# Kernel tuning notes

Hardware: AMD Instinct MI355X
Metric: run time of the kernel (lower is better)

The kernel has to match this reference:

```python
import jax, jax.numpy as jnp
from jax import lax
import numpy as np

VOCAB = 100000
MAX_SEQ = 8192
DIM = 128
K = 5
STRIDE = 1
PAD = 2


def setup_inputs() -> dict:
    key = jax.random.key(0)
    ks = jax.random.split(key, 6)
    X = jax.random.randint(ks[0], (8, 8192), 0, VOCAB, dtype=jnp.int64)
    # nn.Linear(vocab, dim): weight (dim, vocab), bias (dim)
    W_lin = jax.random.normal(ks[1], (DIM, VOCAB), dtype=jnp.float32) * 0.02
    b_lin = jax.random.normal(ks[2], (DIM,), dtype=jnp.float32) * 0.02
    # nn.Conv1d(dim, dim, k): weight (out=dim, in=dim, k), bias (dim)
    W_conv = jax.random.normal(ks[3], (DIM, DIM, K), dtype=jnp.float32) * 0.02
    b_conv = jax.random.normal(ks[4], (DIM,), dtype=jnp.float32) * 0.02
    # nn.Embedding(max_seq_len, dim)
    pos_table = jax.random.normal(ks[5], (MAX_SEQ, DIM), dtype=jnp.float32) * 0.02
    return {"X": X, "W_lin": W_lin, "b_lin": b_lin,
            "W_conv": W_conv, "b_conv": b_conv, "pos_table": pos_table}


def reference(X, W_lin, b_lin, W_conv, b_conv, pos_table):
    # one_hot(X) @ W_lin.T + b_lin  ==  gather rows of W_lin.T
    emb = jnp.take(W_lin.T, X, axis=0) + b_lin          # (b, n, d)
    x = jnp.transpose(emb, (0, 2, 1))                   # (b, d, n)
    y = lax.conv_general_dilated(
        x, W_conv, window_strides=(STRIDE,), padding=[(PAD, PAD)],
        dimension_numbers=("NCH", "OIH", "NCH"))
    y = y + b_conv[None, :, None]                       # (b, d, n_out)
    tokens = jnp.transpose(y, (0, 2, 1))                # (b, n_out, d)
    n_out = tokens.shape[1]
    return tokens + pos_table[:n_out][None, :, :]
```

## Files before the change

### kernel.cpp

```cpp
#include <hip/hip_runtime.h>
#include <hip/hip_bf16.h>
#include <stdint.h>

#define VOCAB 100000
#define SEQ   8192
#define BATCH 8
#define DIM   128

typedef short bf16x8 __attribute__((ext_vector_type(8)));
typedef float f32x4  __attribute__((ext_vector_type(4)));

__device__ __forceinline__ ushort f2bf(float f) {
  union { float f; uint32_t u; } v; v.f = f;
  uint32_t u = v.u;
  return (ushort)((u + 0x7FFF + ((u >> 16) & 1)) >> 16);
}

__global__ void repack_wconv(const float* __restrict__ wconv,
                             ushort* __restrict__ wcb) {
  int e = blockIdx.x * 256 + threadIdx.x;
  if (e >= 5 * DIM * DIM) return;
  int k = e / (DIM * DIM);
  int rem = e % (DIM * DIM);
  int d = rem / DIM, i = rem % DIM;
  wcb[e] = f2bf(wconv[(d * DIM + i) * 5 + k]);
}

__global__ __launch_bounds__(256) void build_wlt(
    const float* __restrict__ wlin, const float* __restrict__ blin,
    ushort* __restrict__ wlt) {
  __shared__ float tile[128 * 65];
  const int tid = threadIdx.x;
  const int t0  = blockIdx.x * 64;

  const int c4 = (tid & 15) * 4;
  const int rbase = tid >> 4;
  const bool cvalid = (t0 + c4) < VOCAB;
#pragma unroll
  for (int p = 0; p < 8; ++p) {
    int r = p * 16 + rbase;
    float4 v = make_float4(0.f, 0.f, 0.f, 0.f);
    if (cvalid) v = *(const float4*)(wlin + (size_t)r * VOCAB + t0 + c4);
    float* dst = &tile[r * 65 + c4];
    dst[0] = v.x; dst[1] = v.y; dst[2] = v.z; dst[3] = v.w;
  }
  __syncthreads();

  const int chunk = tid & 15;
  float bias8[8];
#pragma unroll
  for (int j = 0; j < 8; ++j) bias8[j] = blin[chunk * 8 + j];

#pragma unroll
  for (int p = 0; p < 4; ++p) {
    int tl = (tid >> 4) + p * 16;
    int t  = t0 + tl;
    if (t >= VOCAB) continue;
    ushort u[8];
#pragma unroll
    for (int j = 0; j < 8; ++j) {
      float f = tile[(chunk * 8 + j) * 65 + tl] + bias8[j];
      u[j] = f2bf(f);
    }
    *(uint4*)(wlt + (size_t)t * DIM + chunk * 8) = *(const uint4*)u;
  }
}

__global__ __launch_bounds__(256, 2) void conv_main(
    const int* __restrict__ X, const ushort* __restrict__ wlt,
    const ushort* __restrict__ wcb, const float* __restrict__ bconv,
    const float* __restrict__ pos, float* __restrict__ out) {
  __shared__ __align__(16) ushort Atile[132 * 136];

  const int tid   = threadIdx.x;
  const int bm    = blockIdx.x;
  const int batch = bm >> 6;
  const int nbase = (bm & 63) << 7;
  const int* Xb   = X + batch * SEQ;

  int  tok[9];
  bool valid[9];
#pragma unroll
  for (int it = 0; it < 9; ++it) {
    int c = tid + it * 256;
    int r = c >> 4;
    int n = nbase - 2 + r;
    bool v = (c < 2112) && (n >= 0) && (n < SEQ);
    valid[it] = v;
    tok[it] = v ? Xb[n] : 0;
  }
  uint4 val[9];
#pragma unroll
  for (int it = 0; it < 9; ++it) {
    int c = tid + it * 256;
    int ch = c & 15;
    val[it] = valid[it] ? *(const uint4*)(wlt + (size_t)tok[it] * DIM + ch * 8)
                        : make_uint4(0u, 0u, 0u, 0u);
  }
#pragma unroll
  for (int it = 0; it < 9; ++it) {
    int c = tid + it * 256;
    if (c < 2112) {
      int r = c >> 4, ch = c & 15;
      *(uint4*)&Atile[r * 136 + ch * 8] = val[it];
    }
  }
  __syncthreads();

  const int wave = tid >> 6;
  const int lane = tid & 63;
  const int wm = (wave >> 1) << 6;
  const int wn = (wave & 1) << 6;
  const int lr = lane & 15;
  const int lq = lane >> 4;

  f32x4 acc[4][4];
#pragma unroll
  for (int a = 0; a < 4; ++a)
#pragma unroll
    for (int b = 0; b < 4; ++b) acc[a][b] = (f32x4)0.f;

#pragma unroll
  for (int k = 0; k < 5; ++k) {
    bf16x8 B[4][4];
#pragma unroll
    for (int nt = 0; nt < 4; ++nt)
#pragma unroll
      for (int kk = 0; kk < 4; ++kk)
        B[nt][kk] = *(const bf16x8*)(wcb +
            ((size_t)(k * DIM + wn + nt * 16 + lr) * DIM + kk * 32 + lq * 8));
#pragma unroll
    for (int kk = 0; kk < 4; ++kk) {
      bf16x8 A[4];
#pragma unroll
      for (int mt = 0; mt < 4; ++mt)
        A[mt] = *(const bf16x8*)&Atile[(wm + mt * 16 + lr + k) * 136 + kk * 32 + lq * 8];
#pragma unroll
      for (int mt = 0; mt < 4; ++mt)
#pragma unroll
        for (int nt = 0; nt < 4; ++nt)
          acc[mt][nt] = __builtin_amdgcn_mfma_f32_16x16x32_bf16(
              A[mt], B[nt][kk], acc[mt][nt], 0, 0, 0);
    }
  }

  float bc[4];
#pragma unroll
  for (int nt = 0; nt < 4; ++nt) bc[nt] = bconv[wn + nt * 16 + lr];
  float* outb = out + (size_t)batch * SEQ * DIM;
#pragma unroll
  for (int mt = 0; mt < 4; ++mt) {
#pragma unroll
    for (int rr = 0; rr < 4; ++rr) {
      int m = wm + mt * 16 + lq * 4 + rr;
      int gn = nbase + m;
      const float* posrow = pos + (size_t)gn * DIM;
      float* orow = outb + (size_t)gn * DIM;
#pragma unroll
      for (int nt = 0; nt < 4; ++nt) {
        int d = wn + nt * 16 + lr;
        orow[d] = acc[mt][nt][rr] + bc[nt] + posrow[d];
      }
    }
  }
}

extern "C" void kernel_launch(void* const* d_in, const int* in_sizes, int n_in,
                              void* d_out, int out_size, void* d_ws, size_t ws_size,
                              hipStream_t stream) {
  const int*   X     = (const int*)d_in[0];
  const float* wlin  = (const float*)d_in[1];
  const float* blin  = (const float*)d_in[2];
  const float* wconv = (const float*)d_in[3];
  const float* bconv = (const float*)d_in[4];
  const float* pos   = (const float*)d_in[5];
  float*       out   = (float*)d_out;

  ushort* wcb = (ushort*)d_ws;
  ushort* wlt = (ushort*)((char*)d_ws + 262144);

  hipLaunchKernelGGL(repack_wconv, dim3(320), dim3(256), 0, stream, wconv, wcb);
  hipLaunchKernelGGL(build_wlt, dim3((VOCAB + 63) / 64), dim3(256), 0, stream,
                     wlin, blin, wlt);
  hipLaunchKernelGGL(conv_main, dim3(512), dim3(256), 0, stream,
                     X, wlt, wcb, bconv, pos, out);
}
```

Measured before the change: 144.6 us.

## Merge prep kernels and halve conv tile rows for more blocks and occupancy

Merges the wconv repack and the W_lin transpose kernels into one launch, with extra blocks handling the repack. The main conv kernel now uses 64-row tiles instead of 128, so it launches 1024 blocks with a smaller LDS tile and higher launch-bounds occupancy. B fragments are loaded per kk step rather than all at once, which reduces register pressure. The cost is more halo overhead per block (68 rows for 64 outputs) and more repeated loads of the conv weights.

```diff
diff --git a/kernel.cpp b/kernel.cpp
--- a/kernel.cpp
+++ b/kernel.cpp
@@ -6,6 +6,9 @@
 #define SEQ   8192
 #define BATCH 8
 #define DIM   128
+
+#define WLT_BLOCKS 1563
+#define WCONV_BLOCKS 320
 
 typedef short bf16x8 __attribute__((ext_vector_type(8)));
 typedef float f32x4  __attribute__((ext_vector_type(4)));
@@ -16,22 +19,23 @@
   return (ushort)((u + 0x7FFF + ((u >> 16) & 1)) >> 16);
 }
 
-__global__ void repack_wconv(const float* __restrict__ wconv,
-                             ushort* __restrict__ wcb) {
-  int e = blockIdx.x * 256 + threadIdx.x;
-  if (e >= 5 * DIM * DIM) return;
-  int k = e / (DIM * DIM);
-  int rem = e % (DIM * DIM);
-  int d = rem / DIM, i = rem % DIM;
-  wcb[e] = f2bf(wconv[(d * DIM + i) * 5 + k]);
-}
-
-__global__ __launch_bounds__(256) void build_wlt(
+__global__ __launch_bounds__(256) void prep(
     const float* __restrict__ wlin, const float* __restrict__ blin,
-    ushort* __restrict__ wlt) {
+    const float* __restrict__ wconv, ushort* __restrict__ wlt,
+    ushort* __restrict__ wcb) {
   __shared__ float tile[128 * 65];
   const int tid = threadIdx.x;
-  const int t0  = blockIdx.x * 64;
+
+  if (blockIdx.x >= WLT_BLOCKS) {
+    int e = (blockIdx.x - WLT_BLOCKS) * 256 + tid;
+    int k = e / (DIM * DIM);
+    int rem = e % (DIM * DIM);
+    int d = rem / DIM, i = rem % DIM;
+    wcb[e] = f2bf(wconv[(d * DIM + i) * 5 + k]);
+    return;
+  }
+
+  const int t0 = blockIdx.x * 64;
 
   const int c4 = (tid & 15) * 4;
   const int rbase = tid >> 4;
@@ -58,49 +62,46 @@
     if (t >= VOCAB) continue;
     ushort u[8];
 #pragma unroll
-    for (int j = 0; j < 8; ++j) {
-      float f = tile[(chunk * 8 + j) * 65 + tl] + bias8[j];
-      u[j] = f2bf(f);
-    }
+    for (int j = 0; j < 8; ++j)
+      u[j] = f2bf(tile[(chunk * 8 + j) * 65 + tl] + bias8[j]);
     *(uint4*)(wlt + (size_t)t * DIM + chunk * 8) = *(const uint4*)u;
   }
 }
 
-__global__ __launch_bounds__(256, 2) void conv_main(
+__global__ __launch_bounds__(256, 4) void conv_main(
     const int* __restrict__ X, const ushort* __restrict__ wlt,
     const ushort* __restrict__ wcb, const float* __restrict__ bconv,
     const float* __restrict__ pos, float* __restrict__ out) {
-  __shared__ __align__(16) ushort Atile[132 * 136];
+  __shared__ __align__(16) ushort Atile[68 * 136];
 
   const int tid   = threadIdx.x;
   const int bm    = blockIdx.x;
-  const int batch = bm >> 6;
-  const int nbase = (bm & 63) << 7;
+  const int batch = bm >> 7;
+  const int nbase = (bm & 127) << 6;
   const int* Xb   = X + batch * SEQ;
 
-  int  tok[9];
-  bool valid[9];
+  int  tok[5];
+  bool valid[5];
 #pragma unroll
-  for (int it = 0; it < 9; ++it) {
+  for (int it = 0; it < 5; ++it) {
     int c = tid + it * 256;
     int r = c >> 4;
     int n = nbase - 2 + r;
-    bool v = (c < 2112) && (n >= 0) && (n < SEQ);
+    bool v = (c < 1088) && (n >= 0) && (n < SEQ);
     valid[it] = v;
     tok[it] = v ? Xb[n] : 0;
   }
-  uint4 val[9];
+  uint4 val[5];
 #pragma unroll
-  for (int it = 0; it < 9; ++it) {
-    int c = tid + it * 256;
-    int ch = c & 15;
+  for (int it = 0; it < 5; ++it) {
+    int ch = (tid + it * 256) & 15;
     val[it] = valid[it] ? *(const uint4*)(wlt + (size_t)tok[it] * DIM + ch * 8)
                         : make_uint4(0u, 0u, 0u, 0u);
   }
 #pragma unroll
-  for (int it = 0; it < 9; ++it) {
+  for (int it = 0; it < 5; ++it) {
     int c = tid + it * 256;
-    if (c < 2112) {
+    if (c < 1088) {
       int r = c >> 4, ch = c & 15;
       *(uint4*)&Atile[r * 136 + ch * 8] = val[it];
     }
@@ -109,38 +110,36 @@
 
   const int wave = tid >> 6;
   const int lane = tid & 63;
-  const int wm = (wave >> 1) << 6;
+  const int wm = (wave >> 1) << 5;
   const int wn = (wave & 1) << 6;
   const int lr = lane & 15;
   const int lq = lane >> 4;
 
-  f32x4 acc[4][4];
+  f32x4 acc[2][4];
 #pragma unroll
-  for (int a = 0; a < 4; ++a)
+  for (int a = 0; a < 2; ++a)
 #pragma unroll
     for (int b = 0; b < 4; ++b) acc[a][b] = (f32x4)0.f;
 
 #pragma unroll
   for (int k = 0; k < 5; ++k) {
-    bf16x8 B[4][4];
-#pragma unroll
-    for (int nt = 0; nt < 4; ++nt)
-#pragma unroll
-      for (int kk = 0; kk < 4; ++kk)
-        B[nt][kk] = *(const bf16x8*)(wcb +
-            ((size_t)(k * DIM + wn + nt * 16 + lr) * DIM + kk * 32 + lq * 8));
 #pragma unroll
     for (int kk = 0; kk < 4; ++kk) {
-      bf16x8 A[4];
+      bf16x8 B[4];
 #pragma unroll
-      for (int mt = 0; mt < 4; ++mt)
+      for (int nt = 0; nt < 4; ++nt)
+        B[nt] = *(const bf16x8*)(wcb +
+            ((size_t)(k * DIM + wn + nt * 16 + lr) * DIM + kk * 32 + lq * 8));
+      bf16x8 A[2];
+#pragma unroll
+      for (int mt = 0; mt < 2; ++mt)
         A[mt] = *(const bf16x8*)&Atile[(wm + mt * 16 + lr + k) * 136 + kk * 32 + lq * 8];
 #pragma unroll
-      for (int mt = 0; mt < 4; ++mt)
+      for (int mt = 0; mt < 2; ++mt)
 #pragma unroll
         for (int nt = 0; nt < 4; ++nt)
           acc[mt][nt] = __builtin_amdgcn_mfma_f32_16x16x32_bf16(
-              A[mt], B[nt][kk], acc[mt][nt], 0, 0, 0);
+              A[mt], B[nt], acc[mt][nt], 0, 0, 0);
     }
   }
 
@@ -149,7 +148,7 @@
   for (int nt = 0; nt < 4; ++nt) bc[nt] = bconv[wn + nt * 16 + lr];
   float* outb = out + (size_t)batch * SEQ * DIM;
 #pragma unroll
-  for (int mt = 0; mt < 4; ++mt) {
+  for (int mt = 0; mt < 2; ++mt) {
 #pragma unroll
     for (int rr = 0; rr < 4; ++rr) {
       int m = wm + mt * 16 + lq * 4 + rr;
@@ -179,9 +178,8 @@
   ushort* wcb = (ushort*)d_ws;
   ushort* wlt = (ushort*)((char*)d_ws + 262144);
 
-  hipLaunchKernelGGL(repack_wconv, dim3(320), dim3(256), 0, stream, wconv, wcb);
-  hipLaunchKernelGGL(build_wlt, dim3((VOCAB + 63) / 64), dim3(256), 0, stream,
-                     wlin, blin, wlt);
-  hipLaunchKernelGGL(conv_main, dim3(512), dim3(256), 0, stream,
+  hipLaunchKernelGGL(prep, dim3(WLT_BLOCKS + WCONV_BLOCKS), dim3(256), 0, stream,
+                     wlin, blin, wconv, wlt, wcb);
+  hipLaunchKernelGGL(conv_main, dim3(1024), dim3(256), 0, stream,
                      X, wlt, wcb, bconv, pos, out);
 }
```

After: 154.6 us. 6.9% more time.
